# Optimization experiments

Hardware: AMD Instinct MI355X
Metric: run time of the kernel (lower is better)

Reference implementation:

```python
import jax, jax.numpy as jnp
import numpy as np

# SphericalFilter constants (hardcoded in __init__: num_basis=5, max_center=3.5)
NUM_BASIS = 5
MAX_CENTER = 3.5
SPREAD = MAX_CENTER / NUM_BASIS  # 0.7
CENTERS = jnp.linspace(0.0, MAX_CENTER, NUM_BASIS)  # [5]


def solid_harmonics(edges, l_f):
    """Real solid harmonics of displacement vectors. l=0 -> [1], l=1 -> (x,y,z)."""
    if l_f == 0:
        return jnp.ones(edges.shape[:-1] + (1,), dtype=edges.dtype)
    return edges  # l_f == 1


def spherical_filter(edges, coeffs, l_f):
    """edges: [E,3], coeffs: [C, NUM_BASIS] -> [E, C, 2*l_f+1]."""
    r = jnp.linalg.norm(edges, axis=-1)                              # [E]
    rbf = jnp.exp(-SPREAD * (r[:, None] - CENTERS[None, :]) ** 2)    # [E, B]
    rad = jnp.einsum('eb,cb->ec', rbf, coeffs)                       # [E, C]
    y = solid_harmonics(edges, l_f)                                  # [E, 2lf+1]
    return rad[:, :, None] * y[:, None, :]                           # [E, C, 2lf+1]


def setup_inputs() -> dict:
    key = jax.random.key(0)
    N, E, C = 20000, 320000, 32
    ks = jax.random.split(key, 16)
    inp = {
        'nodes0': jax.random.normal(ks[0], (N, C, 1), dtype=jnp.float32),
        'nodes1': jax.random.normal(ks[1], (N, C, 3), dtype=jnp.float32),
        'edges': jax.random.normal(ks[2], (E, 3), dtype=jnp.float32),
        'senders': jax.random.randint(ks[3], (E,), 0, N, dtype=jnp.int32),
        'receivers': jax.random.randint(ks[4], (E,), 0, N, dtype=jnp.int32),
        # SphericalFilter coeffs per (l, l_f) pair: [C, NUM_BASIS]
        'coeffs_0_0': jax.random.normal(ks[5], (C, NUM_BASIS), dtype=jnp.float32),
        'coeffs_0_1': jax.random.normal(ks[6], (C, NUM_BASIS), dtype=jnp.float32),
        'coeffs_1_0': jax.random.normal(ks[7], (C, NUM_BASIS), dtype=jnp.float32),
        'coeffs_1_1': jax.random.normal(ks[8], (C, NUM_BASIS), dtype=jnp.float32),
        # depthwise tensor-product weights per (l, l_f, l_o): [C]
        'w_0_0_0': jax.random.normal(ks[9], (C,), dtype=jnp.float32),
        'w_0_1_1': jax.random.normal(ks[10], (C,), dtype=jnp.float32),
        'w_1_0_1': jax.random.normal(ks[11], (C,), dtype=jnp.float32),
        'w_1_1_0': jax.random.normal(ks[12], (C,), dtype=jnp.float32),
        'w_1_1_1': jax.random.normal(ks[13], (C,), dtype=jnp.float32),
    }
    return inp


def reference(nodes0, nodes1, edges, senders, receivers,
              coeffs_0_0, coeffs_0_1, coeffs_1_0, coeffs_1_1,
              w_0_0_0, w_0_1_1, w_1_0_1, w_1_1_0, w_1_1_1):
    N = nodes0.shape[0]
    # gather node features by sender (edge-wise)
    n0 = nodes0[senders]  # [E, C, 1]
    n1 = nodes1[senders]  # [E, C, 3]
    # spherical filters on displacements
    f00 = spherical_filter(edges, coeffs_0_0, 0)  # [E, C, 1]  (l=0, l_f=0)
    f01 = spherical_filter(edges, coeffs_0_1, 1)  # [E, C, 3]  (l=0, l_f=1)
    f10 = spherical_filter(edges, coeffs_1_0, 0)  # [E, C, 1]  (l=1, l_f=0)
    f11 = spherical_filter(edges, coeffs_1_1, 1)  # [E, C, 3]  (l=1, l_f=1)
    # depthwise Clebsch-Gordan tensor products (real basis, l_max=1)
    m_000 = w_0_0_0[:, None] * (n0 * f00)                                        # 0x0->0: [E,C,1]
    m_011 = w_0_1_1[:, None] * (n0 * f01)                                        # 0x1->1: [E,C,3]
    m_101 = w_1_0_1[:, None] * (n1 * f10)                                        # 1x0->1: [E,C,3]
    m_110 = w_1_1_0[:, None] * (jnp.sum(n1 * f11, axis=-1, keepdims=True)
                                / jnp.sqrt(3.0))                                 # 1x1->0: [E,C,1]
    m_111 = w_1_1_1[:, None] * (jnp.cross(n1, f11) / jnp.sqrt(2.0))              # 1x1->1: [E,C,3]
    # concatenate messages per output degree along channel axis (-2),
    # in iteration order: l=0 filters [0,1] then l=1 filters [0,1]
    msg0 = jnp.concatenate([m_000, m_110], axis=-2)         # [E, 2C, 1]
    msg1 = jnp.concatenate([m_011, m_101, m_111], axis=-2)  # [E, 3C, 3]
    # scatter-sum into receiver nodes
    out0 = jax.ops.segment_sum(msg0, receivers, num_segments=N)  # [N, 2C, 1]
    out1 = jax.ops.segment_sum(msg1, receivers, num_segments=N)  # [N, 3C, 3]
    return out0, out1
```

## Files before the change

### kernel.cpp

```cpp
#include <hip/hip_runtime.h>
#include <hip/hip_fp16.h>
#include <stdint.h>

#define CCH 32
#define NB 5
#define INV_SQRT3 0.5773502691896258f
#define INV_SQRT2 0.7071067811865476f
#define SPREAD 0.7f
#define CSTEP 0.875f
#define GEXP 1.225f
#define CAP 64

typedef float f32x4 __attribute__((ext_vector_type(4)));

__device__ __constant__ float KB[NB] = {
    1.0f, 0.58512492f, 0.11721312f, 0.0080390154f, 1.8876653e-4f
};


__global__ __launch_bounds__(256) void scatter_kernel(
    const int*   __restrict__ receivers,
    const int*   __restrict__ senders,
    const float* __restrict__ edges,
    int*         __restrict__ counts,
    f32x4*       __restrict__ recs,
    int E, int cap)
{
    int i = blockIdx.x * blockDim.x + threadIdx.x;
    if (i >= E) return;
    int r = receivers[i];
    int pos = atomicAdd(&counts[r], 1);
    if (pos >= cap) return;
    float ex = edges[3 * i + 0];
    float ey = edges[3 * i + 1];
    float ez = edges[3 * i + 2];
    float rr = sqrtf(ex * ex + ey * ey + ez * ez);
    rr = fminf(rr, 12.0f);
    float A = __expf(-SPREAD * rr * rr);
    float g = __expf(GEXP * rr);

    unsigned int hx = __half_as_ushort(__float2half(ex));
    unsigned int hy = __half_as_ushort(__float2half(ey));
    unsigned int hz = __half_as_ushort(__float2half(ez));
    unsigned int w0 = hx | (hy << 16);
    unsigned int w1 = hz | ((unsigned int)senders[i] << 16);

    f32x4 rec;
    rec.x = A;
    rec.y = g;
    rec.z = __uint_as_float(w0);
    rec.w = __uint_as_float(w1);
    recs[(size_t)r * CAP + pos] = rec;
}


__device__ __forceinline__ void tp_accum(
    const f32x4 rec, float n0, float n1x, float n1y, float n1z,
    const float* kp00, const float* kp01, const float* kp10, const float* kp11,
    float& acc000, float& acc110,
    float& a011x, float& a011y, float& a011z,
    float& a101x, float& a101y, float& a101z,
    float& a111x, float& a111y, float& a111z)
{
    float A = rec.x;
    float g = rec.y;
    unsigned int w0 = __float_as_uint(rec.z);
    unsigned int w1 = __float_as_uint(rec.w);
    float ex = __half2float(__ushort_as_half((unsigned short)(w0 & 0xffffu)));
    float ey = __half2float(__ushort_as_half((unsigned short)(w0 >> 16)));
    float ez = __half2float(__ushort_as_half((unsigned short)(w1 & 0xffffu)));

    float p00 = kp00[4], p01 = kp01[4], p10 = kp10[4], p11 = kp11[4];
    #pragma unroll
    for (int b = 3; b >= 0; --b) {
        p00 = fmaf(p00, g, kp00[b]);
        p01 = fmaf(p01, g, kp01[b]);
        p10 = fmaf(p10, g, kp10[b]);
        p11 = fmaf(p11, g, kp11[b]);
    }
    float rad00 = A * p00;
    float rad01 = A * p01;
    float rad10 = A * p10;
    float rad11 = A * p11;

    acc000 = fmaf(n0, rad00, acc000);
    float t01 = n0 * rad01;
    a011x = fmaf(t01, ex, a011x);
    a011y = fmaf(t01, ey, a011y);
    a011z = fmaf(t01, ez, a011z);
    a101x = fmaf(rad10, n1x, a101x);
    a101y = fmaf(rad10, n1y, a101y);
    a101z = fmaf(rad10, n1z, a101z);
    float dotp = n1x * ex + n1y * ey + n1z * ez;
    acc110 = fmaf(rad11, dotp, acc110);
    float cx = n1y * ez - n1z * ey;
    float cy = n1z * ex - n1x * ez;
    float cz = n1x * ey - n1y * ex;
    a111x = fmaf(rad11, cx, a111x);
    a111y = fmaf(rad11, cy, a111y);
    a111z = fmaf(rad11, cz, a111z);
}

__global__ __launch_bounds__(256) void tp_node_kernel(
    const float* __restrict__ nodes0,
    const float* __restrict__ nodes1,
    const int*   __restrict__ counts,
    const f32x4* __restrict__ recs,
    const float* __restrict__ c00,
    const float* __restrict__ c01,
    const float* __restrict__ c10,
    const float* __restrict__ c11,
    const float* __restrict__ w000,
    const float* __restrict__ w011,
    const float* __restrict__ w101,
    const float* __restrict__ w110,
    const float* __restrict__ w111,
    float* __restrict__ out0,
    float* __restrict__ out1,
    int N, int cap)
{
    int n = blockIdx.x * 4 + (threadIdx.x >> 6);
    int lane = threadIdx.x & 63;
    int h = lane >> 5;
    int c = lane & 31;
    if (n >= N) return;

    float kp00[NB], kp01[NB], kp10[NB], kp11[NB];
    #pragma unroll
    for (int b = 0; b < NB; ++b) {
        kp00[b] = c00[c * NB + b] * KB[b];
        kp01[b] = c01[c * NB + b] * KB[b];
        kp10[b] = c10[c * NB + b] * KB[b];
        kp11[b] = c11[c * NB + b] * KB[b];
    }

    int cnt = counts[n];
    if (cnt > cap) cnt = cap;
    const f32x4* bucket = recs + (size_t)n * CAP;

    float acc000 = 0.f, acc110 = 0.f;
    float a011x = 0.f, a011y = 0.f, a011z = 0.f;
    float a101x = 0.f, a101y = 0.f, a101z = 0.f;
    float a111x = 0.f, a111y = 0.f, a111z = 0.f;

    int ii = h;
    for (; ii + 2 < cnt; ii += 4) {
        f32x4 rA = bucket[ii];
        f32x4 rB = bucket[ii + 2];
        int sA = (int)(__float_as_uint(rA.w) >> 16);
        int sB = (int)(__float_as_uint(rB.w) >> 16);
        float n0A  = nodes0[sA * CCH + c];
        float n1Ax = nodes1[(sA * CCH + c) * 3 + 0];
        float n1Ay = nodes1[(sA * CCH + c) * 3 + 1];
        float n1Az = nodes1[(sA * CCH + c) * 3 + 2];
        float n0B  = nodes0[sB * CCH + c];
        float n1Bx = nodes1[(sB * CCH + c) * 3 + 0];
        float n1By = nodes1[(sB * CCH + c) * 3 + 1];
        float n1Bz = nodes1[(sB * CCH + c) * 3 + 2];
        tp_accum(rA, n0A, n1Ax, n1Ay, n1Az,
                 kp00, kp01, kp10, kp11,
                 acc000, acc110, a011x, a011y, a011z,
                 a101x, a101y, a101z, a111x, a111y, a111z);
        tp_accum(rB, n0B, n1Bx, n1By, n1Bz,
                 kp00, kp01, kp10, kp11,
                 acc000, acc110, a011x, a011y, a011z,
                 a101x, a101y, a101z, a111x, a111y, a111z);
    }
    for (; ii < cnt; ii += 2) {
        f32x4 rA = bucket[ii];
        int sA = (int)(__float_as_uint(rA.w) >> 16);
        float n0A  = nodes0[sA * CCH + c];
        float n1Ax = nodes1[(sA * CCH + c) * 3 + 0];
        float n1Ay = nodes1[(sA * CCH + c) * 3 + 1];
        float n1Az = nodes1[(sA * CCH + c) * 3 + 2];
        tp_accum(rA, n0A, n1Ax, n1Ay, n1Az,
                 kp00, kp01, kp10, kp11,
                 acc000, acc110, a011x, a011y, a011z,
                 a101x, a101y, a101z, a111x, a111y, a111z);
    }

    acc000 += __shfl_xor(acc000, 32, 64);
    acc110 += __shfl_xor(acc110, 32, 64);
    a011x += __shfl_xor(a011x, 32, 64);
    a011y += __shfl_xor(a011y, 32, 64);
    a011z += __shfl_xor(a011z, 32, 64);
    a101x += __shfl_xor(a101x, 32, 64);
    a101y += __shfl_xor(a101y, 32, 64);
    a101z += __shfl_xor(a101z, 32, 64);
    a111x += __shfl_xor(a111x, 32, 64);
    a111y += __shfl_xor(a111y, 32, 64);
    a111z += __shfl_xor(a111z, 32, 64);

    if (h == 0) {
        float W000 = w000[c];
        float W011 = w011[c];
        float W101 = w101[c];
        float W110 = w110[c] * INV_SQRT3;
        float W111 = w111[c] * INV_SQRT2;

        float* o0 = out0 + (size_t)n * (2 * CCH);
        o0[c]       = W000 * acc000;
        o0[CCH + c] = W110 * acc110;

        float* o1 = out1 + (size_t)n * (3 * CCH) * 3;
        o1[(c) * 3 + 0] = W011 * a011x;
        o1[(c) * 3 + 1] = W011 * a011y;
        o1[(c) * 3 + 2] = W011 * a011z;
        o1[(CCH + c) * 3 + 0] = W101 * a101x;
        o1[(CCH + c) * 3 + 1] = W101 * a101y;
        o1[(CCH + c) * 3 + 2] = W101 * a101z;
        o1[(2 * CCH + c) * 3 + 0] = W111 * a111x;
        o1[(2 * CCH + c) * 3 + 1] = W111 * a111y;
        o1[(2 * CCH + c) * 3 + 2] = W111 * a111z;
    }
}

extern "C" void kernel_launch(void* const* d_in, const int* in_sizes, int n_in,
                              void* d_out, int out_size, void* d_ws, size_t ws_size,
                              hipStream_t stream) {
    const float* nodes0    = (const float*)d_in[0];
    const float* nodes1    = (const float*)d_in[1];
    const float* edges     = (const float*)d_in[2];
    const int*   senders   = (const int*)d_in[3];
    const int*   receivers = (const int*)d_in[4];
    const float* c00       = (const float*)d_in[5];
    const float* c01       = (const float*)d_in[6];
    const float* c10       = (const float*)d_in[7];
    const float* c11       = (const float*)d_in[8];
    const float* w000      = (const float*)d_in[9];
    const float* w011      = (const float*)d_in[10];
    const float* w101      = (const float*)d_in[11];
    const float* w110      = (const float*)d_in[12];
    const float* w111      = (const float*)d_in[13];

    int N = in_sizes[0] / CCH;
    int E = in_sizes[2] / 3;

    float* out0 = (float*)d_out;
    float* out1 = out0 + (size_t)N * 2 * CCH;

    int* counts = (int*)d_ws;
    f32x4* recs = (f32x4*)((char*)d_ws + (size_t)N * sizeof(int));

    size_t avail = ws_size - (size_t)N * sizeof(int);
    int cap = (int)(avail / ((size_t)N * sizeof(f32x4)));
    if (cap > CAP) cap = CAP;

    (void)hipMemsetAsync(counts, 0, (size_t)N * sizeof(int), stream);

    int sblocks = (E + 255) / 256;
    scatter_kernel<<<sblocks, 256, 0, stream>>>(receivers, senders, edges,
                                                counts, recs, E, cap);

    int blocks = (N + 3) / 4;
    tp_node_kernel<<<blocks, 256, 0, stream>>>(
        nodes0, nodes1, counts, recs,
        c00, c01, c10, c11,
        w000, w011, w101, w110, w111,
        out0, out1, N, cap);
}
```

Baseline: 72.22 us.

## Pack node features into fp16 uint2 and fold counts reset into pack kernel

Adds a pre-pass kernel that converts nodes0 and nodes1 per (node, channel) into four fp16 values packed into one 8-byte word. The gather kernel then does one 8-byte load per sender instead of four scattered fp32 loads, which cuts gather bandwidth. The same pre-pass zeroes the counts array in place of the memset, and the bucket stride now uses the runtime cap. The cost is an extra pass over the node arrays and reduced precision of node features.

```diff
diff --git a/kernel.cpp b/kernel.cpp
--- a/kernel.cpp
+++ b/kernel.cpp
@@ -16,6 +16,32 @@
 __device__ __constant__ float KB[NB] = {
     1.0f, 0.58512492f, 0.11721312f, 0.0080390154f, 1.8876653e-4f
 };
+
+__device__ __forceinline__ float lo16f(unsigned int u) {
+    return __half2float(__ushort_as_half((unsigned short)(u & 0xffffu)));
+}
+__device__ __forceinline__ float hi16f(unsigned int u) {
+    return __half2float(__ushort_as_half((unsigned short)(u >> 16)));
+}
+
+
+__global__ __launch_bounds__(256) void pack_nodes_kernel(
+    const float* __restrict__ nodes0, const float* __restrict__ nodes1,
+    uint2* __restrict__ nPack, int* __restrict__ counts, int N, int total)
+{
+    int i = blockIdx.x * blockDim.x + threadIdx.x;
+    if (i >= total) return;
+    if (i < N) counts[i] = 0;
+    float n0  = nodes0[i];
+    float n1x = nodes1[i * 3 + 0];
+    float n1y = nodes1[i * 3 + 1];
+    float n1z = nodes1[i * 3 + 2];
+    unsigned int w0 = (unsigned int)__half_as_ushort(__float2half(n0))
+                    | ((unsigned int)__half_as_ushort(__float2half(n1x)) << 16);
+    unsigned int w1 = (unsigned int)__half_as_ushort(__float2half(n1y))
+                    | ((unsigned int)__half_as_ushort(__float2half(n1z)) << 16);
+    nPack[i] = make_uint2(w0, w1);
+}
 
 
 __global__ __launch_bounds__(256) void scatter_kernel(
@@ -50,12 +76,12 @@
     rec.y = g;
     rec.z = __uint_as_float(w0);
     rec.w = __uint_as_float(w1);
-    recs[(size_t)r * CAP + pos] = rec;
+    recs[(size_t)r * cap + pos] = rec;
 }
 
 
 __device__ __forceinline__ void tp_accum(
-    const f32x4 rec, float n0, float n1x, float n1y, float n1z,
+    const f32x4 rec, uint2 pk,
     const float* kp00, const float* kp01, const float* kp10, const float* kp11,
     float& acc000, float& acc110,
     float& a011x, float& a011y, float& a011z,
@@ -66,9 +92,14 @@
     float g = rec.y;
     unsigned int w0 = __float_as_uint(rec.z);
     unsigned int w1 = __float_as_uint(rec.w);
-    float ex = __half2float(__ushort_as_half((unsigned short)(w0 & 0xffffu)));
-    float ey = __half2float(__ushort_as_half((unsigned short)(w0 >> 16)));
-    float ez = __half2float(__ushort_as_half((unsigned short)(w1 & 0xffffu)));
+    float ex = lo16f(w0);
+    float ey = hi16f(w0);
+    float ez = lo16f(w1);
+
+    float n0  = lo16f(pk.x);
+    float n1x = hi16f(pk.x);
+    float n1y = lo16f(pk.y);
+    float n1z = hi16f(pk.y);
 
     float p00 = kp00[4], p01 = kp01[4], p10 = kp10[4], p11 = kp11[4];
     #pragma unroll
@@ -102,8 +133,7 @@
 }
 
 __global__ __launch_bounds__(256) void tp_node_kernel(
-    const float* __restrict__ nodes0,
-    const float* __restrict__ nodes1,
+    const uint2* __restrict__ nPack,
     const int*   __restrict__ counts,
     const f32x4* __restrict__ recs,
     const float* __restrict__ c00,
@@ -136,7 +166,7 @@
 
     int cnt = counts[n];
     if (cnt > cap) cnt = cap;
-    const f32x4* bucket = recs + (size_t)n * CAP;
+    const f32x4* bucket = recs + (size_t)n * cap;
 
     float acc000 = 0.f, acc110 = 0.f;
     float a011x = 0.f, a011y = 0.f, a011z = 0.f;
@@ -149,32 +179,20 @@
         f32x4 rB = bucket[ii + 2];
         int sA = (int)(__float_as_uint(rA.w) >> 16);
         int sB = (int)(__float_as_uint(rB.w) >> 16);
-        float n0A  = nodes0[sA * CCH + c];
-        float n1Ax = nodes1[(sA * CCH + c) * 3 + 0];
-        float n1Ay = nodes1[(sA * CCH + c) * 3 + 1];
-        float n1Az = nodes1[(sA * CCH + c) * 3 + 2];
-        float n0B  = nodes0[sB * CCH + c];
-        float n1Bx = nodes1[(sB * CCH + c) * 3 + 0];
-        float n1By = nodes1[(sB * CCH + c) * 3 + 1];
-        float n1Bz = nodes1[(sB * CCH + c) * 3 + 2];
-        tp_accum(rA, n0A, n1Ax, n1Ay, n1Az,
-                 kp00, kp01, kp10, kp11,
+        uint2 pA = nPack[sA * CCH + c];
+        uint2 pB = nPack[sB * CCH + c];
+        tp_accum(rA, pA, kp00, kp01, kp10, kp11,
                  acc000, acc110, a011x, a011y, a011z,
                  a101x, a101y, a101z, a111x, a111y, a111z);
-        tp_accum(rB, n0B, n1Bx, n1By, n1Bz,
-                 kp00, kp01, kp10, kp11,
+        tp_accum(rB, pB, kp00, kp01, kp10, kp11,
                  acc000, acc110, a011x, a011y, a011z,
                  a101x, a101y, a101z, a111x, a111y, a111z);
     }
     for (; ii < cnt; ii += 2) {
         f32x4 rA = bucket[ii];
         int sA = (int)(__float_as_uint(rA.w) >> 16);
-        float n0A  = nodes0[sA * CCH + c];
-        float n1Ax = nodes1[(sA * CCH + c) * 3 + 0];
-        float n1Ay = nodes1[(sA * CCH + c) * 3 + 1];
-        float n1Az = nodes1[(sA * CCH + c) * 3 + 2];
-        tp_accum(rA, n0A, n1Ax, n1Ay, n1Az,
-                 kp00, kp01, kp10, kp11,
+        uint2 pA = nPack[sA * CCH + c];
+        tp_accum(rA, pA, kp00, kp01, kp10, kp11,
                  acc000, acc110, a011x, a011y, a011z,
                  a101x, a101y, a101z, a111x, a111y, a111z);
     }
@@ -239,14 +257,19 @@
     float* out0 = (float*)d_out;
     float* out1 = out0 + (size_t)N * 2 * CCH;
 
-    int* counts = (int*)d_ws;
-    f32x4* recs = (f32x4*)((char*)d_ws + (size_t)N * sizeof(int));
-
-    size_t avail = ws_size - (size_t)N * sizeof(int);
+    char* p = (char*)d_ws;
+    int* counts  = (int*)p;              p += (size_t)N * sizeof(int);
+    uint2* nPack = (uint2*)p;            p += (size_t)N * CCH * sizeof(uint2);
+    f32x4* recs  = (f32x4*)p;
+
+    size_t used = (size_t)(p - (char*)d_ws);
+    size_t avail = (ws_size > used) ? (ws_size - used) : 0;
     int cap = (int)(avail / ((size_t)N * sizeof(f32x4)));
     if (cap > CAP) cap = CAP;
 
-    (void)hipMemsetAsync(counts, 0, (size_t)N * sizeof(int), stream);
+    int ptotal = N * CCH;
+    pack_nodes_kernel<<<(ptotal + 255) / 256, 256, 0, stream>>>(
+        nodes0, nodes1, nPack, counts, N, ptotal);
 
     int sblocks = (E + 255) / 256;
     scatter_kernel<<<sblocks, 256, 0, stream>>>(receivers, senders, edges,
@@ -254,7 +277,7 @@
 
     int blocks = (N + 3) / 4;
     tp_node_kernel<<<blocks, 256, 0, stream>>>(
-        nodes0, nodes1, counts, recs,
+        nPack, counts, recs,
         c00, c01, c10, c11,
         w000, w011, w101, w110, w111,
         out0, out1, N, cap);
```

Result: faster. 59.38 us (-17.8%).
